# Optimization experiments

Hardware: AMD Instinct MI355X
Metric: run time of the kernel (lower is better)

Reference implementation:

```python
import jax, jax.numpy as jnp
import numpy as np

N, E, G = 100000, 1600000, 8
IN, H, OUT = 3, 64, 20


def setup_inputs() -> dict:
    key = jax.random.key(0)
    ks = jax.random.split(key, 24)
    def nrm(k, shape, scale=0.1):
        return jax.random.normal(k, shape, dtype=jnp.float32) * scale
    inp = {}
    inp["x"] = jax.random.normal(ks[0], (N, IN), dtype=jnp.float32)
    inp["edge_index"] = jax.random.randint(ks[1], (2, E), 0, N, dtype=jnp.int32)
    inp["batch"] = jnp.sort(jax.random.randint(ks[2], (N,), 0, G, dtype=jnp.int32))
    dims = [(IN, H), (H, H), (H, H)]  # 3 GATConv layers (initial + layers-1)
    for i, (di, do) in enumerate(dims):
        inp[f"W{i}"] = nrm(ks[3 + 4 * i], (di, do))
        inp[f"as{i}"] = nrm(ks[4 + 4 * i], (do,))
        inp[f"ad{i}"] = nrm(ks[5 + 4 * i], (do,))
        inp[f"b{i}"] = jnp.zeros((do,), jnp.float32)
    inp["vn_emb0"] = jnp.zeros((1, H), jnp.float32)  # constant-0 init per module
    inp["m1_w1"] = nrm(ks[15], (H, H)); inp["m1_b1"] = jnp.zeros((H,), jnp.float32)
    inp["m1_w2"] = nrm(ks[16], (H, H)); inp["m1_b2"] = jnp.zeros((H,), jnp.float32)
    inp["mf_w1"] = nrm(ks[17], (H, H)); inp["mf_b1"] = jnp.zeros((H,), jnp.float32)
    inp["mf_w2"] = nrm(ks[18], (H, OUT)); inp["mf_b2"] = jnp.zeros((OUT,), jnp.float32)
    inp["out_w"] = nrm(ks[19], (H, OUT)); inp["out_b"] = jnp.zeros((OUT,), jnp.float32)
    return inp


def _gat(x, src, dst, W, a_s, a_d, b):
    # PyG GATConv, 1 head: h = xW; e_ij = LeakyReLU_0.2(a_s.h_j + a_d.h_i);
    # alpha = softmax over incoming edges of each dst node; out_i = sum_j alpha_ij h_j + b
    h = x @ W                                                  # [N, H]
    lg = jax.nn.leaky_relu((h @ a_s)[src] + (h @ a_d)[dst], 0.2)  # [E+N]
    m = jax.ops.segment_max(lg, dst, num_segments=N)
    m = jnp.where(jnp.isfinite(m), m, 0.0)
    p = jnp.exp(lg - m[dst])
    denom = jax.ops.segment_sum(p, dst, num_segments=N)
    alpha = p / denom[dst]
    return jax.ops.segment_sum(alpha[:, None] * h[src], dst, num_segments=N) + b


def _forward(x, edge_index, batch, params):
    (W0, as0, ad0, b0, W1, as1, ad1, b1, W2, as2, ad2, b2,
     vn_emb0, m1_w1, m1_b1, m1_w2, m1_b2, mf_w1, mf_b1, mf_w2, mf_b2,
     out_w, out_b) = params
    loops = jnp.arange(N, dtype=edge_index.dtype)  # GATConv add_self_loops=True
    src = jnp.concatenate([edge_index[0], loops])
    dst = jnp.concatenate([edge_index[1], loops])
    act = lambda v: jax.nn.leaky_relu(v, 0.01)  # nn.LeakyReLU default slope
    h = act(_gat(x, src, dst, W0, as0, ad0, b0))
    h = act(_gat(h, src, dst, W1, as1, ad1, b1))
    h = act(_gat(h, src, dst, W2, as2, ad2, b2))
    # virtual node: global_add_pool(out, batch) + Embedding(0) (zero-init)
    vn = jax.ops.segment_sum(h, batch, num_segments=G) + vn_emb0[0]
    vn = jax.nn.relu(vn @ m1_w1 + m1_b1)
    vn = jax.nn.relu(vn @ m1_w2 + m1_b2)
    vn = jax.nn.relu(vn @ mf_w1 + mf_b1)
    vn = jax.nn.relu(vn @ mf_w2 + mf_b2)
    return (h @ out_w + out_b, vn)


def reference(x, edge_index, batch, W0, as0, ad0, b0, W1, as1, ad1, b1,
              W2, as2, ad2, b2, vn_emb0, m1_w1, m1_b1, m1_w2, m1_b2,
              mf_w1, mf_b1, mf_w2, mf_b2, out_w, out_b):
    params = (W0, as0, ad0, b0, W1, as1, ad1, b1, W2, as2, ad2, b2,
              vn_emb0, m1_w1, m1_b1, m1_w2, m1_b2, mf_w1, mf_b1, mf_w2, mf_b2,
              out_w, out_b)
    return _forward(x, edge_index, batch, params)
```

## Files before the change

### kernel.cpp

```cpp
#include <hip/hip_runtime.h>
#include <hip/hip_bf16.h>

#define H 64
#define OUTD 20
#define NGRAPH 8
#define CAP 64
#define NBK 256
#define CAPB 8192

typedef __attribute__((ext_vector_type(8))) short bf16x8;
typedef __attribute__((ext_vector_type(4))) float f32x4;
typedef __attribute__((ext_vector_type(8))) unsigned short u16x8;

__device__ __forceinline__ float ldp(const void* p, int i, bool f32) {
    return f32 ? ((const float*)p)[i]
               : __bfloat162float(((const __hip_bfloat16*)p)[i]);
}

__device__ __forceinline__ float bfu(unsigned short u) {
    union { unsigned int i; float f; } c; c.i = ((unsigned)u) << 16; return c.f;
}
__device__ __forceinline__ unsigned short fbits(float f) {
    __hip_bfloat16 b = __float2bfloat16(f);
    return *reinterpret_cast<unsigned short*>(&b);
}

__global__ void detect_dtype(const unsigned short* __restrict__ xb, int n_u16,
                             int* __restrict__ flag) {
    __shared__ int sh[256];
    int t = threadIdx.x;
    int m = min(n_u16, 4096);
    int bad = 0;
    for (int i = t; i < m; i += 256) {
        unsigned e = (xb[i] >> 7) & 0xFF;
        bad += (e >= 0x90) ? 1 : 0;
    }
    sh[t] = bad;
    __syncthreads();
    for (int off = 128; off; off >>= 1) {
        if (t < off) sh[t] += sh[t + off];
        __syncthreads();
    }
    if (t == 0) *flag = (sh[0] > (m >> 4)) ? 1 : 0;
}


__global__ void fillC_dense0(const int* __restrict__ src, const int* __restrict__ dst,
                             int* __restrict__ gcur, unsigned* __restrict__ ebuf,
                             int E, int n, int nC, int EPC, int nbk,
                             const void* __restrict__ x, const void* __restrict__ W,
                             const void* __restrict__ a_s, const void* __restrict__ a_d,
                             __hip_bfloat16* __restrict__ h, float* __restrict__ s,
                             float* __restrict__ d, const int* __restrict__ flagp) {
    if ((int)blockIdx.x < nC) {
        __shared__ unsigned lcnt[NBK];
        __shared__ int lbase[NBK];
        int t = threadIdx.x;
        for (int i = t; i < NBK; i += 256) lcnt[i] = 0;
        __syncthreads();
        int base = blockIdx.x * (256 * EPC) + t;
        for (int i = 0; i < EPC; ++i) {
            int e = base + i * 256;
            if (e < E) {
                int dn = dst[e];
                if ((unsigned)dn < (unsigned)n) atomicAdd(&lcnt[dn >> 9], 1u);
            }
        }
        __syncthreads();
        for (int i = t; i < nbk; i += 256) {
            unsigned c = lcnt[i];
            lbase[i] = c ? atomicAdd(&gcur[i], (int)c) : 0;
            lcnt[i] = 0;
        }
        __syncthreads();
        for (int i = 0; i < EPC; ++i) {
            int e = base + i * 256;
            if (e < E) {
                int dn = dst[e];
                if ((unsigned)dn < (unsigned)n) {
                    int b = dn >> 9;
                    unsigned pos = (unsigned)lbase[b] + atomicAdd(&lcnt[b], 1u);
                    if (pos < CAPB)
                        ebuf[(size_t)b * CAPB + pos] =
                            ((unsigned)src[e] << 9) | (unsigned)(dn & 511);
                }
            }
        }
        return;
    }
    const bool f32 = (*flagp != 0);
    int idx = ((int)blockIdx.x - nC) * 256 + threadIdx.x;
    int node = idx >> 6;
    int f = idx & 63;
    if (node >= n) return;
    float acc = 0.f;
    for (int k = 0; k < 3; ++k)
        acc += ldp(x, node * 3 + k, f32) * ldp(W, k * H + f, f32);
    h[(size_t)node * H + f] = __float2bfloat16(acc);
    float sv = acc * ldp(a_s, f, f32);
    float dv = acc * ldp(a_d, f, f32);
    for (int off = 32; off; off >>= 1) {
        sv += __shfl_xor(sv, off);
        dv += __shfl_xor(dv, off);
    }
    if (f == 0) { s[node] = sv; d[node] = dv; }
}

__global__ __launch_bounds__(512) void bucketD(const unsigned* __restrict__ ebuf,
                                               const int* __restrict__ gcur,
                                               int* __restrict__ cnt,
                                               int* __restrict__ col, int n) {
    __shared__ unsigned lcnt[512];
    int b = blockIdx.x, t = threadIdx.x;
    lcnt[t] = 0;
    __syncthreads();
    int end = min(gcur[b], CAPB);
    const unsigned* reg = ebuf + (size_t)b * CAPB;
    for (int i = t; i < end; i += 512) {
        unsigned e = reg[i];
        int loc = (int)(e & 511u);
        int sn = (int)(e >> 9);
        unsigned pos = atomicAdd(&lcnt[loc], 1u);
        if (pos < CAP) col[(size_t)((b << 9) + loc) * CAP + pos] = sn;
    }
    __syncthreads();
    int node = (b << 9) + t;
    if (node < n) cnt[node] = (int)min(lcnt[t], (unsigned)CAP);
}


__global__ __launch_bounds__(256) void denseN_mfma(
    const __hip_bfloat16* __restrict__ in,
    const void* __restrict__ W,
    const void* __restrict__ a_s, const void* __restrict__ a_d,
    __hip_bfloat16* __restrict__ h, float* __restrict__ s,
    float* __restrict__ d, int n, const int* __restrict__ flagp) {
    const bool f32 = (*flagp != 0);
    __shared__ short Wt[64 * 72];
    int t = threadIdx.x;
    for (int i = t; i < 4096; i += 256) {
        int k = i >> 6, nf = i & 63;
        Wt[nf * 72 + k] = (short)fbits(ldp(W, i, f32));
    }
    __syncthreads();

    int wid = t >> 6, lane = t & 63;
    int quad = lane >> 4, n16 = lane & 15;
    int nodeBase = blockIdx.x * 64 + wid * 16;
    int mrow = nodeBase + n16;
    int mclamp = min(mrow, n - 1);
    const short* inp = (const short*)in;
    const short* arow = inp + (size_t)mclamp * 64;
    bf16x8 a0 = *(const bf16x8*)(arow + quad * 8);
    bf16x8 a1 = *(const bf16x8*)(arow + 32 + quad * 8);

    float as_v[4], ad_v[4];
    for (int nt = 0; nt < 4; ++nt) {
        as_v[nt] = ldp(a_s, nt * 16 + n16, f32);
        ad_v[nt] = ldp(a_d, nt * 16 + n16, f32);
    }

    float sv[4] = {0.f, 0.f, 0.f, 0.f}, dv[4] = {0.f, 0.f, 0.f, 0.f};
    f32x4 accs[4];
    for (int nt = 0; nt < 4; ++nt) {
        const short* wrow = Wt + (nt * 16 + n16) * 72;
        bf16x8 b0 = *(const bf16x8*)(wrow + quad * 8);
        bf16x8 b1 = *(const bf16x8*)(wrow + 32 + quad * 8);
        f32x4 c = {0.f, 0.f, 0.f, 0.f};
        c = __builtin_amdgcn_mfma_f32_16x16x32_bf16(a0, b0, c, 0, 0, 0);
        c = __builtin_amdgcn_mfma_f32_16x16x32_bf16(a1, b1, c, 0, 0, 0);
        accs[nt] = c;
        for (int r = 0; r < 4; ++r) {
            sv[r] += c[r] * as_v[nt];
            dv[r] += c[r] * ad_v[nt];
        }
    }

    for (int r = 0; r < 4; ++r) {
        int node = nodeBase + quad * 4 + r;
        if (node < n) {
            __hip_bfloat16* hr = h + (size_t)node * 64;
            for (int nt = 0; nt < 4; ++nt)
                hr[nt * 16 + n16] = __float2bfloat16(accs[nt][r]);
        }
    }
    for (int r = 0; r < 4; ++r) {
        for (int mask = 1; mask < 16; mask <<= 1) {
            sv[r] += __shfl_xor(sv[r], mask);
            dv[r] += __shfl_xor(dv[r], mask);
        }
    }
    if (n16 == 0) {
        for (int r = 0; r < 4; ++r) {
            int node = nodeBase + quad * 4 + r;
            if (node < n) { s[node] = sv[r]; d[node] = dv[r]; }
        }
    }
}


__global__ void gat_aggregate(const __hip_bfloat16* __restrict__ h,
                              const float* __restrict__ s, const float* __restrict__ d,
                              const int* __restrict__ cnt, const int* __restrict__ col,
                              const void* __restrict__ bias,
                              __hip_bfloat16* __restrict__ out, int n,
                              const int* __restrict__ flagp) {
    const bool f32 = (*flagp != 0);
    int node = (blockIdx.x * blockDim.x + threadIdx.x) >> 6;
    if (node >= n) return;
    int lane = threadIdx.x & 63;
    int deg = min(cnt[node], CAP);
    int D = deg + 1;
    size_t base = (size_t)node * CAP;
    float di = d[node];

    if (D <= 64) {
        bool act = lane < D;
        int j = (lane < deg) ? col[base + lane] : node;
        j = ((unsigned)j < (unsigned)n) ? j : 0;
        float v = act ? s[j] + di : -INFINITY;
        v = v > 0.f ? v : 0.2f * v;
        float m = v;
        for (int off = 32; off; off >>= 1) m = fmaxf(m, __shfl_xor(m, off));
        float wgt = act ? __expf(v - m) : 0.f;
        float wsum = wgt;
        for (int off = 32; off; off >>= 1) wsum += __shfl_xor(wsum, off);

        const u16x8* h8 = (const u16x8*)h;
        int c = lane & 7, q = lane >> 3;
        float a[8] = {0.f, 0.f, 0.f, 0.f, 0.f, 0.f, 0.f, 0.f};
        int groups = (D + 7) >> 3;
        for (int p = 0; p < groups; ++p) {
            int t = 8 * p + q;
            float wt = __shfl(wgt, t);
            int jt = __shfl(j, t);
            u16x8 hv = h8[jt * 8 + c];
            a[0] += wt * bfu(hv[0]);
            a[1] += wt * bfu(hv[1]);
            a[2] += wt * bfu(hv[2]);
            a[3] += wt * bfu(hv[3]);
            a[4] += wt * bfu(hv[4]);
            a[5] += wt * bfu(hv[5]);
            a[6] += wt * bfu(hv[6]);
            a[7] += wt * bfu(hv[7]);
        }
        for (int i = 0; i < 8; ++i) {
            a[i] += __shfl_xor(a[i], 8);
            a[i] += __shfl_xor(a[i], 16);
            a[i] += __shfl_xor(a[i], 32);
        }
        if (lane < 8) {
            float inv = 1.f / fmaxf(wsum, 1e-20f);
            u16x8 ov;
            for (int i = 0; i < 8; ++i) {
                float o = a[i] * inv + ldp(bias, 8 * c + i, f32);
                o = o > 0.f ? o : 0.01f * o;
                ov[i] = fbits(o);
            }
            ((u16x8*)out)[(size_t)node * 8 + c] = ov;
        }
        return;
    }

    float m = -INFINITY;
    for (int e = lane; e < D; e += 64) {
        int j = (e < deg) ? col[base + e] : node;
        j = ((unsigned)j < (unsigned)n) ? j : 0;
        float v = s[j] + di;
        v = v > 0.f ? v : 0.2f * v;
        m = fmaxf(m, v);
    }
    for (int off = 32; off; off >>= 1) m = fmaxf(m, __shfl_xor(m, off));
    if (!(m > -INFINITY)) m = 0.f;

    float acc = 0.f, wsum = 0.f;
    for (int b = 0; b < D; b += 64) {
        int e = b + lane;
        float w = 0.f;
        int j = 0;
        if (e < D) {
            j = (e < deg) ? col[base + e] : node;
            j = ((unsigned)j < (unsigned)n) ? j : 0;
            float v = s[j] + di;
            v = v > 0.f ? v : 0.2f * v;
            w = __expf(v - m);
        }
        wsum += w;
        int c2 = min(64, D - b);
        for (int t = 0; t < c2; ++t) {
            float wt = __shfl(w, t);
            int jt = __shfl(j, t);
            acc += wt * __bfloat162float(h[(size_t)jt * H + lane]);
        }
    }
    for (int off = 32; off; off >>= 1) wsum += __shfl_xor(wsum, off);

    float o = acc / fmaxf(wsum, 1e-20f) + ldp(bias, lane, f32);
    o = o > 0.f ? o : 0.01f * o;
    out[(size_t)node * H + lane] = __float2bfloat16(o);
}


__global__ __launch_bounds__(256) void proj_pool(
    const __hip_bfloat16* __restrict__ h,
    const void* __restrict__ W, const void* __restrict__ b,
    void* __restrict__ out, int n, const int* __restrict__ flagp,
    int projBlocks, const int* __restrict__ batch, float* __restrict__ vn) {
    const bool f32 = (*flagp != 0);
    if ((int)blockIdx.x < projBlocks) {
        __shared__ short Wt[32 * 72];
        int t = threadIdx.x;
        for (int i = t; i < 32 * 64; i += 256) {
            int o = i >> 6, k = i & 63;
            Wt[o * 72 + k] = (o < OUTD) ? (short)fbits(ldp(W, k * OUTD + o, f32)) : 0;
        }
        __syncthreads();

        int wid = t >> 6, lane = t & 63;
        int quad = lane >> 4, n16 = lane & 15;
        int nodeBase = blockIdx.x * 64 + wid * 16;
        int mclamp = min(nodeBase + n16, n - 1);
        const short* arow = (const short*)h + (size_t)mclamp * 64;
        bf16x8 a0 = *(const bf16x8*)(arow + quad * 8);
        bf16x8 a1 = *(const bf16x8*)(arow + 32 + quad * 8);

        f32x4 acc0 = {0.f, 0.f, 0.f, 0.f}, acc1 = {0.f, 0.f, 0.f, 0.f};
        {
            const short* wrow = Wt + n16 * 72;
            bf16x8 b0 = *(const bf16x8*)(wrow + quad * 8);
            bf16x8 b1 = *(const bf16x8*)(wrow + 32 + quad * 8);
            acc0 = __builtin_amdgcn_mfma_f32_16x16x32_bf16(a0, b0, acc0, 0, 0, 0);
            acc0 = __builtin_amdgcn_mfma_f32_16x16x32_bf16(a1, b1, acc0, 0, 0, 0);
        }
        {
            const short* wrow = Wt + (16 + n16) * 72;
            bf16x8 b0 = *(const bf16x8*)(wrow + quad * 8);
            bf16x8 b1 = *(const bf16x8*)(wrow + 32 + quad * 8);
            acc1 = __builtin_amdgcn_mfma_f32_16x16x32_bf16(a0, b0, acc1, 0, 0, 0);
            acc1 = __builtin_amdgcn_mfma_f32_16x16x32_bf16(a1, b1, acc1, 0, 0, 0);
        }
        float bv0 = ldp(b, n16, f32);
        float bv1 = (n16 < OUTD - 16) ? ldp(b, 16 + n16, f32) : 0.f;
        for (int r = 0; r < 4; ++r) {
            int node = nodeBase + quad * 4 + r;
            if (node >= n) break;
            float o0 = acc0[r] + bv0;
            if (f32) ((float*)out)[node * OUTD + n16] = o0;
            else     ((__hip_bfloat16*)out)[node * OUTD + n16] = __float2bfloat16(o0);
            if (n16 < OUTD - 16) {
                float o1 = acc1[r] + bv1;
                if (f32) ((float*)out)[node * OUTD + 16 + n16] = o1;
                else     ((__hip_bfloat16*)out)[node * OUTD + 16 + n16] = __float2bfloat16(o1);
            }
        }
        return;
    }
    __shared__ float part[NGRAPH * H];
    int t = threadIdx.x;
    for (int i = t; i < NGRAPH * H; i += 256) part[i] = 0.f;
    __syncthreads();
    int pb = (int)blockIdx.x - projBlocks;
    int npb = gridDim.x - projBlocks;
    int wid = t >> 6, lane = t & 63;
    int gwave = pb * 4 + wid;
    int nwaves = npb * 4;
    int chunk = (n + nwaves - 1) / nwaves;
    int beg = gwave * chunk;
    int end = min(n, beg + chunk);
    if (beg < end) {
        float acc = 0.f;
        int cur = batch[beg];
        for (int i = beg; i < end; ++i) {
            int g = batch[i];
            if (g != cur) {
                if ((unsigned)cur < NGRAPH) atomicAdd(&part[cur * H + lane], acc);
                acc = 0.f;
                cur = g;
            }
            acc += __bfloat162float(h[(size_t)i * H + lane]);
        }
        if ((unsigned)cur < NGRAPH) atomicAdd(&part[cur * H + lane], acc);
    }
    __syncthreads();
    for (int i = t; i < NGRAPH * H; i += 256) {
        float v = part[i];
        if (v != 0.f) atomicAdd(&vn[i], v);
    }
}


__global__ void vn_mlp(const float* __restrict__ vn, const void* __restrict__ emb,
                       const void* __restrict__ w1, const void* __restrict__ b1,
                       const void* __restrict__ w2, const void* __restrict__ b2,
                       const void* __restrict__ w3, const void* __restrict__ b3,
                       const void* __restrict__ w4, const void* __restrict__ b4,
                       void* __restrict__ out, int out1_off, const int* __restrict__ flagp) {
    const bool f32 = (*flagp != 0);
    __shared__ float A[NGRAPH * H], B[NGRAPH * H];
    int t = threadIdx.x;
    int g = t >> 6, f = t & 63;
    A[t] = vn[t] + ldp(emb, f, f32);
    __syncthreads();
    float acc = ldp(b1, f, f32);
    for (int k = 0; k < H; ++k) acc += A[g * H + k] * ldp(w1, k * H + f, f32);
    B[t] = fmaxf(acc, 0.f);
    __syncthreads();
    acc = ldp(b2, f, f32);
    for (int k = 0; k < H; ++k) acc += B[g * H + k] * ldp(w2, k * H + f, f32);
    A[t] = fmaxf(acc, 0.f);
    __syncthreads();
    acc = ldp(b3, f, f32);
    for (int k = 0; k < H; ++k) acc += A[g * H + k] * ldp(w3, k * H + f, f32);
    B[t] = fmaxf(acc, 0.f);
    __syncthreads();
    if (f < OUTD) {
        acc = ldp(b4, f, f32);
        for (int k = 0; k < H; ++k) acc += B[g * H + k] * ldp(w4, k * OUTD + f, f32);
        acc = fmaxf(acc, 0.f);
        int idx = out1_off + g * OUTD + f;
        if (f32) ((float*)out)[idx] = acc;
        else     ((__hip_bfloat16*)out)[idx] = __float2bfloat16(acc);
    }
}


extern "C" void kernel_launch(void* const* d_in, const int* in_sizes, int n_in,
                              void* d_out, int out_size, void* d_ws, size_t ws_size,
                              hipStream_t stream) {
    const void* x   = d_in[0];
    const int* ei   = (const int*)d_in[1];
    const int* batch= (const int*)d_in[2];
    const void* W0  = d_in[3];
    const void* as0 = d_in[4];
    const void* ad0 = d_in[5];
    const void* b0  = d_in[6];
    const void* W1  = d_in[7];
    const void* as1 = d_in[8];
    const void* ad1 = d_in[9];
    const void* b1  = d_in[10];
    const void* W2  = d_in[11];
    const void* as2 = d_in[12];
    const void* ad2 = d_in[13];
    const void* b2  = d_in[14];
    const void* vne = d_in[15];
    const void* m1w1 = d_in[16];
    const void* m1b1 = d_in[17];
    const void* m1w2 = d_in[18];
    const void* m1b2 = d_in[19];
    const void* mfw1 = d_in[20];
    const void* mfb1 = d_in[21];
    const void* mfw2 = d_in[22];
    const void* mfb2 = d_in[23];
    const void* outw = d_in[24];
    const void* outb = d_in[25];

    const int N = in_sizes[2];
    const int E = in_sizes[1] / 2;
    const int* srcp = ei;
    const int* dstp = ei + E;

    char* w = (char*)d_ws;
    auto alloc = [&](size_t bytes) -> void* {
        void* p = (void*)w;
        w += ((bytes + 255) / 256) * 256;
        return p;
    };
    int*   flag   = (int*)alloc(256);
    int*   gcur   = (int*)alloc((size_t)NBK * 4);
    unsigned* ebuf= (unsigned*)alloc((size_t)NBK * CAPB * 4);
    int*   cnt    = (int*)alloc((size_t)N * 4);
    int*   col    = (int*)alloc((size_t)N * CAP * 4);
    __hip_bfloat16* featA = (__hip_bfloat16*)alloc((size_t)N * H * 2);
    __hip_bfloat16* featB = (__hip_bfloat16*)alloc((size_t)N * H * 2);
    __hip_bfloat16* hbuf  = (__hip_bfloat16*)alloc((size_t)N * H * 2);
    float* sArr   = (float*)alloc((size_t)N * 4);
    float* dArr   = (float*)alloc((size_t)N * 4);
    float* vn     = (float*)alloc((size_t)NGRAPH * H * 4);

    const int nbN64 = (N * H + 255) / 256;
    const int nb64 = (N + 63) / 64;
    const int projBlocks = (N + 63) / 64;
    const int nbk = (N + 511) >> 9;
    int EPC = 32;
    int nC = (E + 256 * EPC - 1) / (256 * EPC);
    while (nC > 256) { EPC <<= 1; nC = (E + 256 * EPC - 1) / (256 * EPC); }

    detect_dtype<<<1, 256, 0, stream>>>((const unsigned short*)x, in_sizes[0], flag);

    hipMemsetAsync(gcur, 0, (size_t)NBK * 4, stream);
    hipMemsetAsync(vn, 0, (size_t)NGRAPH * H * 4, stream);
    fillC_dense0<<<nC + nbN64, 256, 0, stream>>>(
        srcp, dstp, gcur, ebuf, E, N, nC, EPC, nbk,
        x, W0, as0, ad0, hbuf, sArr, dArr, flag);
    bucketD<<<nbk, 512, 0, stream>>>(ebuf, gcur, cnt, col, N);

    gat_aggregate<<<nbN64, 256, 0, stream>>>(hbuf, sArr, dArr, cnt, col, b0, featA, N, flag);
    denseN_mfma<<<nb64, 256, 0, stream>>>(featA, W1, as1, ad1, hbuf, sArr, dArr, N, flag);
    gat_aggregate<<<nbN64, 256, 0, stream>>>(hbuf, sArr, dArr, cnt, col, b1, featB, N, flag);
    denseN_mfma<<<nb64, 256, 0, stream>>>(featB, W2, as2, ad2, hbuf, sArr, dArr, N, flag);
    gat_aggregate<<<nbN64, 256, 0, stream>>>(hbuf, sArr, dArr, cnt, col, b2, featA, N, flag);

    proj_pool<<<projBlocks + 512, 256, 0, stream>>>(featA, outw, outb, d_out, N, flag,
                                                    projBlocks, batch, vn);
    vn_mlp<<<1, 512, 0, stream>>>(vn, vne, m1w1, m1b1, m1w2, m1b2, mfw1, mfb1, mfw2, mfb2,
                                  d_out, N * OUTD, flag);
}
```

Measured before the change: 426.7 us.

## Fuse GAT aggregation with next-layer dense projection through LDS tiles

Merges each gat_aggregate with the following MFMA projection, and the last aggregation with the output projection and pooling. Each 1024-thread block aggregates 16 nodes into LDS, then one wave runs the MFMA on that tile. This removes the intermediate feature round-trip through global memory and cuts the launch count. Ping-pong buffers are used for h/s/d. The costs are that only one of sixteen waves does the projection and W is reloaded per 16-node block. Pooling now issues global atomics per block instead of staging them in shared memory.

```diff
diff --git a/kernel.cpp b/kernel.cpp
--- a/kernel.cpp
+++ b/kernel.cpp
@@ -129,28 +129,136 @@
 }
 
 
-__global__ __launch_bounds__(256) void denseN_mfma(
-    const __hip_bfloat16* __restrict__ in,
+__device__ __forceinline__ void gat_node_to_lds(
+    int node, int lane, const __hip_bfloat16* __restrict__ h,
+    const float* __restrict__ s, const float* __restrict__ d,
+    const int* __restrict__ cnt, const int* __restrict__ col,
+    const void* __restrict__ bias, bool f32, int n, short* Rrow) {
+    if (node >= n) {
+        if (lane < 8) {
+            u16x8 zz; for (int i = 0; i < 8; ++i) zz[i] = 0;
+            *(u16x8*)(Rrow + lane * 8) = zz;
+        }
+        return;
+    }
+    int deg = min(cnt[node], CAP);
+    int D = deg + 1;
+    size_t base = (size_t)node * CAP;
+    float di = d[node];
+
+    if (D <= 64) {
+        bool act = lane < D;
+        int j = (lane < deg) ? col[base + lane] : node;
+        j = ((unsigned)j < (unsigned)n) ? j : 0;
+        float v = act ? s[j] + di : -INFINITY;
+        v = v > 0.f ? v : 0.2f * v;
+        float m = v;
+        for (int off = 32; off; off >>= 1) m = fmaxf(m, __shfl_xor(m, off));
+        float wgt = act ? __expf(v - m) : 0.f;
+        float wsum = wgt;
+        for (int off = 32; off; off >>= 1) wsum += __shfl_xor(wsum, off);
+
+        const u16x8* h8 = (const u16x8*)h;
+        int c = lane & 7, q = lane >> 3;
+        float a[8] = {0.f, 0.f, 0.f, 0.f, 0.f, 0.f, 0.f, 0.f};
+        int groups = (D + 7) >> 3;
+        for (int p = 0; p < groups; ++p) {
+            int tt = 8 * p + q;
+            float wt = __shfl(wgt, tt);
+            int jt = __shfl(j, tt);
+            u16x8 hv = h8[jt * 8 + c];
+            a[0] += wt * bfu(hv[0]);
+            a[1] += wt * bfu(hv[1]);
+            a[2] += wt * bfu(hv[2]);
+            a[3] += wt * bfu(hv[3]);
+            a[4] += wt * bfu(hv[4]);
+            a[5] += wt * bfu(hv[5]);
+            a[6] += wt * bfu(hv[6]);
+            a[7] += wt * bfu(hv[7]);
+        }
+        for (int i = 0; i < 8; ++i) {
+            a[i] += __shfl_xor(a[i], 8);
+            a[i] += __shfl_xor(a[i], 16);
+            a[i] += __shfl_xor(a[i], 32);
+        }
+        if (lane < 8) {
+            float inv = 1.f / fmaxf(wsum, 1e-20f);
+            u16x8 ov;
+            for (int i = 0; i < 8; ++i) {
+                float o = a[i] * inv + ldp(bias, 8 * c + i, f32);
+                o = o > 0.f ? o : 0.01f * o;
+                ov[i] = fbits(o);
+            }
+            *(u16x8*)(Rrow + c * 8) = ov;
+        }
+        return;
+    }
+
+    float m = -INFINITY;
+    for (int e = lane; e < D; e += 64) {
+        int j = (e < deg) ? col[base + e] : node;
+        j = ((unsigned)j < (unsigned)n) ? j : 0;
+        float v = s[j] + di;
+        v = v > 0.f ? v : 0.2f * v;
+        m = fmaxf(m, v);
+    }
+    for (int off = 32; off; off >>= 1) m = fmaxf(m, __shfl_xor(m, off));
+    if (!(m > -INFINITY)) m = 0.f;
+
+    float acc = 0.f, wsum = 0.f;
+    for (int b = 0; b < D; b += 64) {
+        int e = b + lane;
+        float w = 0.f;
+        int j = 0;
+        if (e < D) {
+            j = (e < deg) ? col[base + e] : node;
+            j = ((unsigned)j < (unsigned)n) ? j : 0;
+            float v = s[j] + di;
+            v = v > 0.f ? v : 0.2f * v;
+            w = __expf(v - m);
+        }
+        wsum += w;
+        int c2 = min(64, D - b);
+        for (int tt = 0; tt < c2; ++tt) {
+            float wt = __shfl(w, tt);
+            int jt = __shfl(j, tt);
+            acc += wt * __bfloat162float(h[(size_t)jt * H + lane]);
+        }
+    }
+    for (int off = 32; off; off >>= 1) wsum += __shfl_xor(wsum, off);
+
+    float o = acc / fmaxf(wsum, 1e-20f) + ldp(bias, lane, f32);
+    o = o > 0.f ? o : 0.01f * o;
+    Rrow[lane] = (short)fbits(o);
+}
+
+
+__global__ __launch_bounds__(1024, 8) void gat_dense(
+    const __hip_bfloat16* __restrict__ h,
+    const float* __restrict__ s, const float* __restrict__ d,
+    const int* __restrict__ cnt, const int* __restrict__ col,
+    const void* __restrict__ bias,
     const void* __restrict__ W,
     const void* __restrict__ a_s, const void* __restrict__ a_d,
-    __hip_bfloat16* __restrict__ h, float* __restrict__ s,
-    float* __restrict__ d, int n, const int* __restrict__ flagp) {
+    __hip_bfloat16* __restrict__ hout, float* __restrict__ sout,
+    float* __restrict__ dout, int n, const int* __restrict__ flagp) {
     const bool f32 = (*flagp != 0);
     __shared__ short Wt[64 * 72];
+    __shared__ short R[16 * 72];
     int t = threadIdx.x;
-    for (int i = t; i < 4096; i += 256) {
+    for (int i = t; i < 4096; i += 1024) {
         int k = i >> 6, nf = i & 63;
         Wt[nf * 72 + k] = (short)fbits(ldp(W, i, f32));
     }
-    __syncthreads();
-
     int wid = t >> 6, lane = t & 63;
+    int blockBase = blockIdx.x * 16;
+    gat_node_to_lds(blockBase + wid, lane, h, s, d, cnt, col, bias, f32, n,
+                    R + wid * 72);
+    __syncthreads();
+
+    if (wid != 0) return;
     int quad = lane >> 4, n16 = lane & 15;
-    int nodeBase = blockIdx.x * 64 + wid * 16;
-    int mrow = nodeBase + n16;
-    int mclamp = min(mrow, n - 1);
-    const short* inp = (const short*)in;
-    const short* arow = inp + (size_t)mclamp * 64;
+    const short* arow = R + n16 * 72;
     bf16x8 a0 = *(const bf16x8*)(arow + quad * 8);
     bf16x8 a1 = *(const bf16x8*)(arow + 32 + quad * 8);
 
@@ -159,7 +267,6 @@
         as_v[nt] = ldp(a_s, nt * 16 + n16, f32);
         ad_v[nt] = ldp(a_d, nt * 16 + n16, f32);
     }
-
     float sv[4] = {0.f, 0.f, 0.f, 0.f}, dv[4] = {0.f, 0.f, 0.f, 0.f};
     f32x4 accs[4];
     for (int nt = 0; nt < 4; ++nt) {
@@ -175,11 +282,10 @@
             dv[r] += c[r] * ad_v[nt];
         }
     }
-
     for (int r = 0; r < 4; ++r) {
-        int node = nodeBase + quad * 4 + r;
+        int node = blockBase + quad * 4 + r;
         if (node < n) {
-            __hip_bfloat16* hr = h + (size_t)node * 64;
+            __hip_bfloat16* hr = hout + (size_t)node * 64;
             for (int nt = 0; nt < 4; ++nt)
                 hr[nt * 16 + n16] = __float2bfloat16(accs[nt][r]);
         }
@@ -192,138 +298,40 @@
     }
     if (n16 == 0) {
         for (int r = 0; r < 4; ++r) {
-            int node = nodeBase + quad * 4 + r;
-            if (node < n) { s[node] = sv[r]; d[node] = dv[r]; }
-        }
-    }
-}
-
-
-__global__ void gat_aggregate(const __hip_bfloat16* __restrict__ h,
-                              const float* __restrict__ s, const float* __restrict__ d,
-                              const int* __restrict__ cnt, const int* __restrict__ col,
-                              const void* __restrict__ bias,
-                              __hip_bfloat16* __restrict__ out, int n,
-                              const int* __restrict__ flagp) {
+            int node = blockBase + quad * 4 + r;
+            if (node < n) { sout[node] = sv[r]; dout[node] = dv[r]; }
+        }
+    }
+}
+
+
+__global__ __launch_bounds__(1024, 8) void gat_proj_pool(
+    const __hip_bfloat16* __restrict__ h,
+    const float* __restrict__ s, const float* __restrict__ d,
+    const int* __restrict__ cnt, const int* __restrict__ col,
+    const void* __restrict__ bias,
+    const void* __restrict__ Wp, const void* __restrict__ bp,
+    void* __restrict__ out, const int* __restrict__ batch,
+    float* __restrict__ vn, int n, const int* __restrict__ flagp) {
     const bool f32 = (*flagp != 0);
-    int node = (blockIdx.x * blockDim.x + threadIdx.x) >> 6;
-    if (node >= n) return;
-    int lane = threadIdx.x & 63;
-    int deg = min(cnt[node], CAP);
-    int D = deg + 1;
-    size_t base = (size_t)node * CAP;
-    float di = d[node];
-
-    if (D <= 64) {
-        bool act = lane < D;
-        int j = (lane < deg) ? col[base + lane] : node;
-        j = ((unsigned)j < (unsigned)n) ? j : 0;
-        float v = act ? s[j] + di : -INFINITY;
-        v = v > 0.f ? v : 0.2f * v;
-        float m = v;
-        for (int off = 32; off; off >>= 1) m = fmaxf(m, __shfl_xor(m, off));
-        float wgt = act ? __expf(v - m) : 0.f;
-        float wsum = wgt;
-        for (int off = 32; off; off >>= 1) wsum += __shfl_xor(wsum, off);
-
-        const u16x8* h8 = (const u16x8*)h;
-        int c = lane & 7, q = lane >> 3;
-        float a[8] = {0.f, 0.f, 0.f, 0.f, 0.f, 0.f, 0.f, 0.f};
-        int groups = (D + 7) >> 3;
-        for (int p = 0; p < groups; ++p) {
-            int t = 8 * p + q;
-            float wt = __shfl(wgt, t);
-            int jt = __shfl(j, t);
-            u16x8 hv = h8[jt * 8 + c];
-            a[0] += wt * bfu(hv[0]);
-            a[1] += wt * bfu(hv[1]);
-            a[2] += wt * bfu(hv[2]);
-            a[3] += wt * bfu(hv[3]);
-            a[4] += wt * bfu(hv[4]);
-            a[5] += wt * bfu(hv[5]);
-            a[6] += wt * bfu(hv[6]);
-            a[7] += wt * bfu(hv[7]);
-        }
-        for (int i = 0; i < 8; ++i) {
-            a[i] += __shfl_xor(a[i], 8);
-            a[i] += __shfl_xor(a[i], 16);
-            a[i] += __shfl_xor(a[i], 32);
-        }
-        if (lane < 8) {
-            float inv = 1.f / fmaxf(wsum, 1e-20f);
-            u16x8 ov;
-            for (int i = 0; i < 8; ++i) {
-                float o = a[i] * inv + ldp(bias, 8 * c + i, f32);
-                o = o > 0.f ? o : 0.01f * o;
-                ov[i] = fbits(o);
-            }
-            ((u16x8*)out)[(size_t)node * 8 + c] = ov;
-        }
-        return;
-    }
-
-    float m = -INFINITY;
-    for (int e = lane; e < D; e += 64) {
-        int j = (e < deg) ? col[base + e] : node;
-        j = ((unsigned)j < (unsigned)n) ? j : 0;
-        float v = s[j] + di;
-        v = v > 0.f ? v : 0.2f * v;
-        m = fmaxf(m, v);
-    }
-    for (int off = 32; off; off >>= 1) m = fmaxf(m, __shfl_xor(m, off));
-    if (!(m > -INFINITY)) m = 0.f;
-
-    float acc = 0.f, wsum = 0.f;
-    for (int b = 0; b < D; b += 64) {
-        int e = b + lane;
-        float w = 0.f;
-        int j = 0;
-        if (e < D) {
-            j = (e < deg) ? col[base + e] : node;
-            j = ((unsigned)j < (unsigned)n) ? j : 0;
-            float v = s[j] + di;
-            v = v > 0.f ? v : 0.2f * v;
-            w = __expf(v - m);
-        }
-        wsum += w;
-        int c2 = min(64, D - b);
-        for (int t = 0; t < c2; ++t) {
-            float wt = __shfl(w, t);
-            int jt = __shfl(j, t);
-            acc += wt * __bfloat162float(h[(size_t)jt * H + lane]);
-        }
-    }
-    for (int off = 32; off; off >>= 1) wsum += __shfl_xor(wsum, off);
-
-    float o = acc / fmaxf(wsum, 1e-20f) + ldp(bias, lane, f32);
-    o = o > 0.f ? o : 0.01f * o;
-    out[(size_t)node * H + lane] = __float2bfloat16(o);
-}
-
-
-__global__ __launch_bounds__(256) void proj_pool(
-    const __hip_bfloat16* __restrict__ h,
-    const void* __restrict__ W, const void* __restrict__ b,
-    void* __restrict__ out, int n, const int* __restrict__ flagp,
-    int projBlocks, const int* __restrict__ batch, float* __restrict__ vn) {
-    const bool f32 = (*flagp != 0);
-    if ((int)blockIdx.x < projBlocks) {
-        __shared__ short Wt[32 * 72];
-        int t = threadIdx.x;
-        for (int i = t; i < 32 * 64; i += 256) {
-            int o = i >> 6, k = i & 63;
-            Wt[o * 72 + k] = (o < OUTD) ? (short)fbits(ldp(W, k * OUTD + o, f32)) : 0;
-        }
-        __syncthreads();
-
-        int wid = t >> 6, lane = t & 63;
+    __shared__ short Wt[32 * 72];
+    __shared__ short R[16 * 72];
+    int t = threadIdx.x;
+    for (int i = t; i < 32 * 64; i += 1024) {
+        int o = i >> 6, k = i & 63;
+        Wt[o * 72 + k] = (o < OUTD) ? (short)fbits(ldp(Wp, k * OUTD + o, f32)) : 0;
+    }
+    int wid = t >> 6, lane = t & 63;
+    int blockBase = blockIdx.x * 16;
+    gat_node_to_lds(blockBase + wid, lane, h, s, d, cnt, col, bias, f32, n,
+                    R + wid * 72);
+    __syncthreads();
+
+    if (wid == 0) {
         int quad = lane >> 4, n16 = lane & 15;
-        int nodeBase = blockIdx.x * 64 + wid * 16;
-        int mclamp = min(nodeBase + n16, n - 1);
-        const short* arow = (const short*)h + (size_t)mclamp * 64;
+        const short* arow = R + n16 * 72;
         bf16x8 a0 = *(const bf16x8*)(arow + quad * 8);
         bf16x8 a1 = *(const bf16x8*)(arow + 32 + quad * 8);
-
         f32x4 acc0 = {0.f, 0.f, 0.f, 0.f}, acc1 = {0.f, 0.f, 0.f, 0.f};
         {
             const short* wrow = Wt + n16 * 72;
@@ -339,10 +347,10 @@
             acc1 = __builtin_amdgcn_mfma_f32_16x16x32_bf16(a0, b0, acc1, 0, 0, 0);
             acc1 = __builtin_amdgcn_mfma_f32_16x16x32_bf16(a1, b1, acc1, 0, 0, 0);
         }
-        float bv0 = ldp(b, n16, f32);
-        float bv1 = (n16 < OUTD - 16) ? ldp(b, 16 + n16, f32) : 0.f;
+        float bv0 = ldp(bp, n16, f32);
+        float bv1 = (n16 < OUTD - 16) ? ldp(bp, 16 + n16, f32) : 0.f;
         for (int r = 0; r < 4; ++r) {
-            int node = nodeBase + quad * 4 + r;
+            int node = blockBase + quad * 4 + r;
             if (node >= n) break;
             float o0 = acc0[r] + bv0;
             if (f32) ((float*)out)[node * OUTD + n16] = o0;
@@ -353,38 +361,21 @@
                 else     ((__hip_bfloat16*)out)[node * OUTD + 16 + n16] = __float2bfloat16(o1);
             }
         }
-        return;
-    }
-    __shared__ float part[NGRAPH * H];
-    int t = threadIdx.x;
-    for (int i = t; i < NGRAPH * H; i += 256) part[i] = 0.f;
-    __syncthreads();
-    int pb = (int)blockIdx.x - projBlocks;
-    int npb = gridDim.x - projBlocks;
-    int wid = t >> 6, lane = t & 63;
-    int gwave = pb * 4 + wid;
-    int nwaves = npb * 4;
-    int chunk = (n + nwaves - 1) / nwaves;
-    int beg = gwave * chunk;
-    int end = min(n, beg + chunk);
-    if (beg < end) {
+    } else if (wid == 1) {
         float acc = 0.f;
-        int cur = batch[beg];
-        for (int i = beg; i < end; ++i) {
-            int g = batch[i];
+        int cur = -1;
+        for (int it = 0; it < 16; ++it) {
+            int node = blockBase + it;
+            if (node >= n) break;
+            int g = batch[node];
             if (g != cur) {
-                if ((unsigned)cur < NGRAPH) atomicAdd(&part[cur * H + lane], acc);
+                if ((unsigned)cur < NGRAPH) atomicAdd(&vn[cur * H + lane], acc);
                 acc = 0.f;
                 cur = g;
             }
-            acc += __bfloat162float(h[(size_t)i * H + lane]);
-        }
-        if ((unsigned)cur < NGRAPH) atomicAdd(&part[cur * H + lane], acc);
-    }
-    __syncthreads();
-    for (int i = t; i < NGRAPH * H; i += 256) {
-        float v = part[i];
-        if (v != 0.f) atomicAdd(&vn[i], v);
+            acc += bfu((unsigned short)R[it * 72 + lane]);
+        }
+        if ((unsigned)cur < NGRAPH) atomicAdd(&vn[cur * H + lane], acc);
     }
 }
 
@@ -470,16 +461,16 @@
     unsigned* ebuf= (unsigned*)alloc((size_t)NBK * CAPB * 4);
     int*   cnt    = (int*)alloc((size_t)N * 4);
     int*   col    = (int*)alloc((size_t)N * CAP * 4);
-    __hip_bfloat16* featA = (__hip_bfloat16*)alloc((size_t)N * H * 2);
-    __hip_bfloat16* featB = (__hip_bfloat16*)alloc((size_t)N * H * 2);
-    __hip_bfloat16* hbuf  = (__hip_bfloat16*)alloc((size_t)N * H * 2);
-    float* sArr   = (float*)alloc((size_t)N * 4);
-    float* dArr   = (float*)alloc((size_t)N * 4);
+    __hip_bfloat16* hA = (__hip_bfloat16*)alloc((size_t)N * H * 2);
+    __hip_bfloat16* hB = (__hip_bfloat16*)alloc((size_t)N * H * 2);
+    float* sA     = (float*)alloc((size_t)N * 4);
+    float* dA     = (float*)alloc((size_t)N * 4);
+    float* sB     = (float*)alloc((size_t)N * 4);
+    float* dB     = (float*)alloc((size_t)N * 4);
     float* vn     = (float*)alloc((size_t)NGRAPH * H * 4);
 
     const int nbN64 = (N * H + 255) / 256;
-    const int nb64 = (N + 63) / 64;
-    const int projBlocks = (N + 63) / 64;
+    const int nb16 = (N + 15) / 16;
     const int nbk = (N + 511) >> 9;
     int EPC = 32;
     int nC = (E + 256 * EPC - 1) / (256 * EPC);
@@ -491,17 +482,15 @@
     hipMemsetAsync(vn, 0, (size_t)NGRAPH * H * 4, stream);
     fillC_dense0<<<nC + nbN64, 256, 0, stream>>>(
         srcp, dstp, gcur, ebuf, E, N, nC, EPC, nbk,
-        x, W0, as0, ad0, hbuf, sArr, dArr, flag);
+        x, W0, as0, ad0, hA, sA, dA, flag);
     bucketD<<<nbk, 512, 0, stream>>>(ebuf, gcur, cnt, col, N);
 
-    gat_aggregate<<<nbN64, 256, 0, stream>>>(hbuf, sArr, dArr, cnt, col, b0, featA, N, flag);
-    denseN_mfma<<<nb64, 256, 0, stream>>>(featA, W1, as1, ad1, hbuf, sArr, dArr, N, flag);
-    gat_aggregate<<<nbN64, 256, 0, stream>>>(hbuf, sArr, dArr, cnt, col, b1, featB, N, flag);
-    denseN_mfma<<<nb64, 256, 0, stream>>>(featB, W2, as2, ad2, hbuf, sArr, dArr, N, flag);
-    gat_aggregate<<<nbN64, 256, 0, stream>>>(hbuf, sArr, dArr, cnt, col, b2, featA, N, flag);
-
-    proj_pool<<<projBlocks + 512, 256, 0, stream>>>(featA, outw, outb, d_out, N, flag,
-                                                    projBlocks, batch, vn);
+    gat_dense<<<nb16, 1024, 0, stream>>>(hA, sA, dA, cnt, col, b0,
+                                         W1, as1, ad1, hB, sB, dB, N, flag);
+    gat_dense<<<nb16, 1024, 0, stream>>>(hB, sB, dB, cnt, col, b1,
+                                         W2, as2, ad2, hA, sA, dA, N, flag);
+    gat_proj_pool<<<nb16, 1024, 0, stream>>>(hA, sA, dA, cnt, col, b2,
+                                             outw, outb, d_out, batch, vn, N, flag);
     vn_mlp<<<1, 512, 0, stream>>>(vn, vne, m1w1, m1b1, m1w2, m1b2, mfw1, mfb1, mfw2, mfb2,
                                   d_out, N * OUTD, flag);
 }
```

Result: slower. 473.1 us (+10.9%).
